# Performance work log

Measured on AMD Instinct MI355X. Metric: run time of the kernel, lower is better.

Reference implementation:

```python
import jax, jax.numpy as jnp
import numpy as np

N, E, G = 50000, 800000, 512
IN, HID, H1, H2, OUT = 128, 32, 8, 4, 128
D1, D2 = HID * H1, HID * H2  # 256, 128


def _ln(x, g, b, eps=1e-5):
    m = x.mean(-1, keepdims=True)
    v = jnp.var(x, axis=-1, keepdims=True)
    return (x - m) * jax.lax.rsqrt(v + eps) * g + b


def _gat_conv(x, W, a_src, a_dst, bias, edge_index, heads, ch, concat):
    # PyG GATConv (eval): h = xW per head; e = leakyrelu(a_src.h_src + a_dst.h_dst);
    # segment softmax over destination nodes; scatter-sum messages; self-loops added.
    n = x.shape[0]
    h = (x @ W).reshape(n, heads, ch)                      # [N,H,C]
    asrc = jnp.sum(h * a_src, axis=-1)                     # [N,H]
    adst = jnp.sum(h * a_dst, axis=-1)                     # [N,H]
    loop = jnp.arange(n)
    src = jnp.concatenate([edge_index[0], loop])           # [E+N]
    dst = jnp.concatenate([edge_index[1], loop])
    e = jax.nn.leaky_relu(asrc[src] + adst[dst], 0.2)      # [E+N,H]
    emax = jax.ops.segment_max(e, dst, num_segments=n)
    p = jnp.exp(e - emax[dst])
    denom = jax.ops.segment_sum(p, dst, num_segments=n)
    alpha = p / (denom[dst] + 1e-16)                       # [E+N,H]
    out = jax.ops.segment_sum(h[src] * alpha[..., None], dst, num_segments=n)  # [N,H,C]
    out = out.reshape(n, heads * ch) if concat else out.mean(axis=1)
    return out + bias


def setup_inputs():
    key = jax.random.key(0)
    ks = jax.random.split(key, 32)
    g = lambda i, shape, s=0.05: jax.random.normal(ks[i], shape, dtype=jnp.float32) * s
    inp = {
        "x": jax.random.normal(ks[0], (N, IN), dtype=jnp.float32),
        "edge_index": jax.random.randint(ks[1], (2, E), 0, N, dtype=jnp.int32),
        "batch": jnp.sort(jax.random.randint(ks[2], (N,), 0, G, dtype=jnp.int32)),
        # GAT layer 1: in 128 -> 8 heads x 32
        "W1": g(3, (IN, H1 * HID)), "a_src1": g(4, (H1, HID)), "a_dst1": g(5, (H1, HID)),
        "b1": jnp.zeros((D1,), jnp.float32), "g1": jnp.ones((D1,), jnp.float32), "be1": jnp.zeros((D1,), jnp.float32),
        "pw1": g(6, (IN, D1)), "pb1": jnp.zeros((D1,), jnp.float32),
        # GAT layer 2: 256 -> 4 heads x 32
        "W2": g(7, (D1, H2 * HID)), "a_src2": g(8, (H2, HID)), "a_dst2": g(9, (H2, HID)),
        "b2": jnp.zeros((D2,), jnp.float32), "g2": jnp.ones((D2,), jnp.float32), "be2": jnp.zeros((D2,), jnp.float32),
        "pw2": g(10, (D1, D2)), "pb2": jnp.zeros((D2,), jnp.float32),
        # GAT layer 3: 128 -> 1 head x 128, concat=False
        "W3": g(11, (D2, OUT)), "a_src3": g(12, (1, OUT)), "a_dst3": g(13, (1, OUT)),
        "b3": jnp.zeros((OUT,), jnp.float32), "g3": jnp.ones((OUT,), jnp.float32), "be3": jnp.zeros((OUT,), jnp.float32),
        "pw3": g(14, (D2, OUT)), "pb3": jnp.zeros((OUT,), jnp.float32),
    }
    return inp


def reference(x, edge_index, batch,
              W1, a_src1, a_dst1, b1, g1, be1, pw1, pb1,
              W2, a_src2, a_dst2, b2, g2, be2, pw2, pb2,
              W3, a_src3, a_dst3, b3, g3, be3, pw3, pb3):
    h1 = _gat_conv(x, W1, a_src1, a_dst1, b1, edge_index, H1, HID, True)
    h1 = jax.nn.elu(_ln(h1, g1, be1) + (x @ pw1 + pb1))
    h2 = _gat_conv(h1, W2, a_src2, a_dst2, b2, edge_index, H2, HID, True)
    h2 = jax.nn.elu(_ln(h2, g2, be2) + (h1 @ pw2 + pb2))
    h3 = _gat_conv(h2, W3, a_src3, a_dst3, b3, edge_index, 1, OUT, False)
    h3 = jax.nn.elu(_ln(h3, g3, be3) + (h2 @ pw3 + pb3))
    # jk='last' -> h3; global mean pool per graph
    sums = jax.ops.segment_sum(h3, batch, num_segments=G)              # [G,OUT]
    cnt = jax.ops.segment_sum(jnp.ones((N,), h3.dtype), batch, num_segments=G)
    return sums / jnp.maximum(cnt, 1.0)[:, None]
```

## Files before the change

kernel.cpp:

```cpp
#include <hip/hip_runtime.h>
#include <hip/hip_fp16.h>
#include <math.h>


typedef _Float16 f16x8 __attribute__((ext_vector_type(8)));
typedef float f32x4 __attribute__((ext_vector_type(4)));

static __device__ __forceinline__ float h2f(unsigned short u) {
  return __half2float(__builtin_bit_cast(__half, u));
}
static __device__ __forceinline__ unsigned short f2h(float f) {
  return __builtin_bit_cast(unsigned short, __float2half_rn(f));
}
static __device__ __forceinline__ float hlo(unsigned int w) {
  return __low2float(__builtin_bit_cast(__half2, w));
}
static __device__ __forceinline__ float hhi(unsigned int w) {
  return __high2float(__builtin_bit_cast(__half2, w));
}
static __device__ __forceinline__ float wave_sum(float v) {
#pragma unroll
  for (int off = 1; off < 64; off <<= 1) v += __shfl_xor(v, off, 64);
  return v;
}

template <int K, int C, int H, bool ATOMIC>
__global__ __launch_bounds__(256) void fused_gemm_kernel(
    const unsigned short* __restrict__ A, const unsigned short* __restrict__ Bp1,
    const unsigned short* __restrict__ Bp2, const float* __restrict__ bias2,
    const float* __restrict__ a_src, const float* __restrict__ a_dst,
    unsigned short* __restrict__ C1, unsigned short* __restrict__ C2,
    float* __restrict__ asrc, float* __restrict__ adst, int Ncols) {
  const int lane = threadIdx.x & 63;
  const int w = threadIdx.x >> 6;
  const int ml = lane & 15, kq = lane >> 4;
  const int row0 = blockIdx.y * 64 + (w >> 1) * 32;
  const int colt0 = blockIdx.x * 4 + (w & 1) * 2;
  constexpr int KB = K / 32;

  f32x4 w00 = {}, w01 = {}, w10 = {}, w11 = {};
  f32x4 p00 = {}, p01 = {}, p10 = {}, p11 = {};
  const unsigned short* a0 = A + (size_t)(row0 + ml) * K + kq * 8;
  const unsigned short* b1 = Bp1 + ((size_t)colt0 * KB * 64 + lane) * 8;
  const unsigned short* b2 = Bp2 + ((size_t)colt0 * KB * 64 + lane) * 8;
#pragma unroll
  for (int kb = 0; kb < KB; kb++) {
    f16x8 af0 = __builtin_bit_cast(f16x8, *(const uint4*)(a0 + kb * 32));
    f16x8 af1 = __builtin_bit_cast(f16x8, *(const uint4*)(a0 + 16 * K + kb * 32));
    f16x8 bw0 = __builtin_bit_cast(f16x8, *(const uint4*)(b1 + (size_t)kb * 512));
    f16x8 bw1 = __builtin_bit_cast(f16x8, *(const uint4*)(b1 + (size_t)(KB + kb) * 512));
    f16x8 bp0 = __builtin_bit_cast(f16x8, *(const uint4*)(b2 + (size_t)kb * 512));
    f16x8 bp1 = __builtin_bit_cast(f16x8, *(const uint4*)(b2 + (size_t)(KB + kb) * 512));
    w00 = __builtin_amdgcn_mfma_f32_16x16x32_f16(af0, bw0, w00, 0, 0, 0);
    w01 = __builtin_amdgcn_mfma_f32_16x16x32_f16(af0, bw1, w01, 0, 0, 0);
    w10 = __builtin_amdgcn_mfma_f32_16x16x32_f16(af1, bw0, w10, 0, 0, 0);
    w11 = __builtin_amdgcn_mfma_f32_16x16x32_f16(af1, bw1, w11, 0, 0, 0);
    p00 = __builtin_amdgcn_mfma_f32_16x16x32_f16(af0, bp0, p00, 0, 0, 0);
    p01 = __builtin_amdgcn_mfma_f32_16x16x32_f16(af0, bp1, p01, 0, 0, 0);
    p10 = __builtin_amdgcn_mfma_f32_16x16x32_f16(af1, bp0, p10, 0, 0, 0);
    p11 = __builtin_amdgcn_mfma_f32_16x16x32_f16(af1, bp1, p11, 0, 0, 0);
  }
  const int c0 = colt0 * 16 + ml, c1 = c0 + 16;
  const float bi0 = bias2[c0], bi1 = bias2[c1];
#pragma unroll
  for (int r = 0; r < 4; r++) {
    const size_t rA = (size_t)(row0 + kq * 4 + r);
    const size_t rB = rA + 16;
    C1[rA * Ncols + c0] = f2h(w00[r]);
    C1[rA * Ncols + c1] = f2h(w01[r]);
    C1[rB * Ncols + c0] = f2h(w10[r]);
    C1[rB * Ncols + c1] = f2h(w11[r]);
    C2[rA * Ncols + c0] = f2h(p00[r] + bi0);
    C2[rA * Ncols + c1] = f2h(p01[r] + bi1);
    C2[rB * Ncols + c0] = f2h(p10[r] + bi0);
    C2[rB * Ncols + c1] = f2h(p11[r] + bi1);
  }

  const int hh = (colt0 * 16) / C;
  const float aS0 = a_src[hh * C + (c0 % C)], aS1 = a_src[hh * C + (c1 % C)];
  const float aD0 = a_dst[hh * C + (c0 % C)], aD1 = a_dst[hh * C + (c1 % C)];
  float pS0[4], pD0[4], pS1[4], pD1[4];
#pragma unroll
  for (int r = 0; r < 4; r++) {
    pS0[r] = w00[r] * aS0 + w01[r] * aS1;
    pD0[r] = w00[r] * aD0 + w01[r] * aD1;
    pS1[r] = w10[r] * aS0 + w11[r] * aS1;
    pD1[r] = w10[r] * aD0 + w11[r] * aD1;
  }
#pragma unroll
  for (int off = 1; off < 16; off <<= 1) {
#pragma unroll
    for (int r = 0; r < 4; r++) {
      pS0[r] += __shfl_xor(pS0[r], off);
      pD0[r] += __shfl_xor(pD0[r], off);
      pS1[r] += __shfl_xor(pS1[r], off);
      pD1[r] += __shfl_xor(pD1[r], off);
    }
  }
  if (ml < 4) {
    const int r = ml;
    const int rowA = row0 + kq * 4 + r;
    const int rowB = rowA + 16;
    if constexpr (ATOMIC) {
      atomicAdd(&asrc[rowA * H + hh], pS0[r]);
      atomicAdd(&adst[rowA * H + hh], pD0[r]);
      atomicAdd(&asrc[rowB * H + hh], pS1[r]);
      atomicAdd(&adst[rowB * H + hh], pD1[r]);
    } else {
      asrc[rowA * H + hh] = pS0[r];
      adst[rowA * H + hh] = pD0[r];
      asrc[rowB * H + hh] = pS1[r];
      adst[rowB * H + hh] = pD1[r];
    }
  }
}

static __device__ __forceinline__ void repack_one(const float* B, unsigned short* Bp,
                                                  int K, int Ncols, int idx) {
  const int KB = K >> 5;
  const int lane = idx & 63;
  const int kb = (idx >> 6) % KB;
  const int nt = idx / (KB << 6);
  const int ml = lane & 15, kq = lane >> 4;
  unsigned short* dst = Bp + (size_t)idx * 8;
#pragma unroll
  for (int j = 0; j < 8; j++)
    dst[j] = f2h(B[(size_t)(kb * 32 + kq * 8 + j) * Ncols + nt * 16 + ml]);
}

__global__ __launch_bounds__(256) void repack_all_kernel(
    const float* W1, const float* pw1, const float* W2, const float* pw2,
    const float* W3, const float* pw3, unsigned short* BpW1, unsigned short* BpP1,
    unsigned short* BpW2, unsigned short* BpP2, unsigned short* BpW3,
    unsigned short* BpP3) {
  int idx = blockIdx.x * 256 + threadIdx.x;
  if (idx < 4096) { repack_one(W1, BpW1, 128, 256, idx); return; }
  idx -= 4096;
  if (idx < 4096) { repack_one(pw1, BpP1, 128, 256, idx); return; }
  idx -= 4096;
  if (idx < 4096) { repack_one(W2, BpW2, 256, 128, idx); return; }
  idx -= 4096;
  if (idx < 4096) { repack_one(pw2, BpP2, 256, 128, idx); return; }
  idx -= 4096;
  if (idx < 2048) { repack_one(W3, BpW3, 128, 128, idx); return; }
  idx -= 2048;
  repack_one(pw3, BpP3, 128, 128, idx);
}

__global__ void cast_f16_kernel(const float* __restrict__ src,
                                unsigned short* __restrict__ dst, int n4, int pad4) {
  const int i = blockIdx.x * 256 + threadIdx.x;
  if (i >= n4 + pad4) return;
  ushort4 o;
  if (i < n4) {
    float4 v = ((const float4*)src)[i];
    o.x = f2h(v.x); o.y = f2h(v.y); o.z = f2h(v.z); o.w = f2h(v.w);
  } else {
    o.x = o.y = o.z = o.w = 0;
  }
  ((ushort4*)dst)[i] = o;
}

__global__ void zero_pads_kernel(unsigned short* b256, unsigned short* b128, int pad) {
  const int i = blockIdx.x * 256 + threadIdx.x;
  if (i < pad * 256) b256[i] = 0;
  if (i < pad * 128) b128[i] = 0;
}

__global__ void zero2_kernel(float* a, float* b, int n) {
  const int i = blockIdx.x * 256 + threadIdx.x;
  if (i < n) { a[i] = 0.f; b[i] = 0.f; }
}

template <int H, int C, int SPLIT>
__global__ __launch_bounds__(256) void gat_agg_kernel(
    const unsigned short* __restrict__ hfeat, const float* __restrict__ asrc,
    const float* __restrict__ adst, const int* __restrict__ rowptr,
    const int* __restrict__ col, const float* __restrict__ bias,
    const float* __restrict__ gamma, const float* __restrict__ beta,
    const unsigned short* __restrict__ proj, unsigned short* __restrict__ out, int N) {
  constexpr int DOUT = H * C;
  constexpr int RL = DOUT / 8;
  constexpr int PD = 4;
  const int wave = threadIdx.x >> 6;
  const int lane = threadIdx.x & 63;
  const int n = blockIdx.x * 4 + wave;
  if (n >= N) return;
  const int rl = lane % RL;
  const int sub = lane / RL;
  const int c0 = rl * 8;
  const int myh = c0 / C;
  const int start = rowptr[n];
  const int deg = rowptr[n + 1] - start;
  const int vlen = deg + 1;
  const float my_adl = adst[n * H + myh];

  float acc[8];
#pragma unroll
  for (int i = 0; i < 8; i++) acc[i] = 0.f;
  float psum = 0.f;
  const __half2 hz = __float2half2_rn(0.f);

  for (int chunk = 0; chunk < vlen; chunk += 64) {
    const int loc = chunk + lane;
    const int cv = (loc < deg) ? col[start + loc] : n;
    const int m = min(64, vlen - chunk);
    const int steps = (m + SPLIT - 1) / SPLIT;
    const int ngroups = (steps + PD - 1) / PD;

    __half2 acc2[4] = {hz, hz, hz, hz};
    float aA[PD], aB[PD];
    uint4 hA[PD], hB[PD];

#pragma unroll
    for (int k = 0; k < PD; k++) {
      const int local = k * SPLIT + sub;
      int s = __shfl(cv, local & 63);
      if (local >= m) s = n;
      aA[k] = asrc[s * H + myh];
      hA[k] = *(const uint4*)&hfeat[(size_t)s * DOUT + c0];
    }
    for (int g = 0; g < ngroups; g += 2) {
      if (g + 1 < ngroups) {
#pragma unroll
        for (int k = 0; k < PD; k++) {
          const int local = ((g + 1) * PD + k) * SPLIT + sub;
          int s = __shfl(cv, local & 63);
          if (local >= m) s = n;
          aB[k] = asrc[s * H + myh];
          hB[k] = *(const uint4*)&hfeat[(size_t)s * DOUT + c0];
        }
      }
#pragma unroll
      for (int k = 0; k < PD; k++) {
        const int local = (g * PD + k) * SPLIT + sub;
        float e = aA[k] + my_adl;
        e = (e > 0.f) ? e : 0.2f * e;
        float p = __expf(e);
        p = (local < m) ? p : 0.f;
        psum += p;
        const __half2 pp = __float2half2_rn(p);
        acc2[0] = __hfma2(__builtin_bit_cast(__half2, hA[k].x), pp, acc2[0]);
        acc2[1] = __hfma2(__builtin_bit_cast(__half2, hA[k].y), pp, acc2[1]);
        acc2[2] = __hfma2(__builtin_bit_cast(__half2, hA[k].z), pp, acc2[2]);
        acc2[3] = __hfma2(__builtin_bit_cast(__half2, hA[k].w), pp, acc2[3]);
      }
      if (g + 1 < ngroups) {
        if (g + 2 < ngroups) {
#pragma unroll
          for (int k = 0; k < PD; k++) {
            const int local = ((g + 2) * PD + k) * SPLIT + sub;
            int s = __shfl(cv, local & 63);
            if (local >= m) s = n;
            aA[k] = asrc[s * H + myh];
            hA[k] = *(const uint4*)&hfeat[(size_t)s * DOUT + c0];
          }
        }
#pragma unroll
        for (int k = 0; k < PD; k++) {
          const int local = ((g + 1) * PD + k) * SPLIT + sub;
          float e = aB[k] + my_adl;
          e = (e > 0.f) ? e : 0.2f * e;
          float p = __expf(e);
          p = (local < m) ? p : 0.f;
          psum += p;
          const __half2 pp = __float2half2_rn(p);
          acc2[0] = __hfma2(__builtin_bit_cast(__half2, hB[k].x), pp, acc2[0]);
          acc2[1] = __hfma2(__builtin_bit_cast(__half2, hB[k].y), pp, acc2[1]);
          acc2[2] = __hfma2(__builtin_bit_cast(__half2, hB[k].z), pp, acc2[2]);
          acc2[3] = __hfma2(__builtin_bit_cast(__half2, hB[k].w), pp, acc2[3]);
        }
      }
    }
#pragma unroll
    for (int i = 0; i < 4; i++) {
      acc[2 * i] += __low2float(acc2[i]);
      acc[2 * i + 1] += __high2float(acc2[i]);
    }
  }

#pragma unroll
  for (int o = RL; o < 64; o <<= 1) {
    psum += __shfl_xor(psum, o);
#pragma unroll
    for (int i = 0; i < 8; i++) acc[i] += __shfl_xor(acc[i], o);
  }

  const float rs = 1.f / (psum + 1e-16f);
  const float4 bi0 = *(const float4*)&bias[c0];
  const float4 bi1 = *(const float4*)&bias[c0 + 4];
  float v[8];
  v[0] = acc[0] * rs + bi0.x; v[1] = acc[1] * rs + bi0.y;
  v[2] = acc[2] * rs + bi0.z; v[3] = acc[3] * rs + bi0.w;
  v[4] = acc[4] * rs + bi1.x; v[5] = acc[5] * rs + bi1.y;
  v[6] = acc[6] * rs + bi1.z; v[7] = acc[7] * rs + bi1.w;

  float s8 = 0.f;
#pragma unroll
  for (int i = 0; i < 8; i++) s8 += v[i];
  const float mean = wave_sum(s8) / (float)(DOUT * SPLIT);
  float q8 = 0.f;
#pragma unroll
  for (int i = 0; i < 8; i++) {
    v[i] -= mean;
    q8 += v[i] * v[i];
  }
  const float var = wave_sum(q8) / (float)(DOUT * SPLIT);
  const float rstd = rsqrtf(var + 1e-5f);

  const float4 ga0 = *(const float4*)&gamma[c0];
  const float4 ga1 = *(const float4*)&gamma[c0 + 4];
  const float4 be0 = *(const float4*)&beta[c0];
  const float4 be1 = *(const float4*)&beta[c0 + 4];
  const uint4 pr = *(const uint4*)&proj[(size_t)n * DOUT + c0];
  float o0 = v[0] * rstd * ga0.x + be0.x + hlo(pr.x);
  float o1 = v[1] * rstd * ga0.y + be0.y + hhi(pr.x);
  float o2 = v[2] * rstd * ga0.z + be0.z + hlo(pr.y);
  float o3 = v[3] * rstd * ga0.w + be0.w + hhi(pr.y);
  float o4 = v[4] * rstd * ga1.x + be1.x + hlo(pr.z);
  float o5 = v[5] * rstd * ga1.y + be1.y + hhi(pr.z);
  float o6 = v[6] * rstd * ga1.z + be1.z + hlo(pr.w);
  float o7 = v[7] * rstd * ga1.w + be1.w + hhi(pr.w);
  o0 = (o0 > 0.f) ? o0 : expm1f(o0);
  o1 = (o1 > 0.f) ? o1 : expm1f(o1);
  o2 = (o2 > 0.f) ? o2 : expm1f(o2);
  o3 = (o3 > 0.f) ? o3 : expm1f(o3);
  o4 = (o4 > 0.f) ? o4 : expm1f(o4);
  o5 = (o5 > 0.f) ? o5 : expm1f(o5);
  o6 = (o6 > 0.f) ? o6 : expm1f(o6);
  o7 = (o7 > 0.f) ? o7 : expm1f(o7);
  if (sub == 0) {
    uint4 ov;
    ov.x = (unsigned int)f2h(o0) | ((unsigned int)f2h(o1) << 16);
    ov.y = (unsigned int)f2h(o2) | ((unsigned int)f2h(o3) << 16);
    ov.z = (unsigned int)f2h(o4) | ((unsigned int)f2h(o5) << 16);
    ov.w = (unsigned int)f2h(o6) | ((unsigned int)f2h(o7) << 16);
    *(uint4*)&out[(size_t)n * DOUT + c0] = ov;
  }
}

__global__ void hist_kernel(const int* __restrict__ dst, int* __restrict__ cnt, int E) {
  const int e = blockIdx.x * 256 + threadIdx.x;
  if (e < E) atomicAdd(&cnt[dst[e]], 1);
}

__global__ __launch_bounds__(256) void scan1_kernel(int* __restrict__ cnt,
                                                    int* __restrict__ sums, int N) {
  __shared__ int sm[256];
  const int i = blockIdx.x * 256 + threadIdx.x;
  const int v = (i < N) ? cnt[i] : 0;
  sm[threadIdx.x] = v;
  __syncthreads();
  for (int off = 1; off < 256; off <<= 1) {
    const int t = (threadIdx.x >= off) ? sm[threadIdx.x - off] : 0;
    __syncthreads();
    sm[threadIdx.x] += t;
    __syncthreads();
  }
  if (i < N) cnt[i] = sm[threadIdx.x] - v;
  if (threadIdx.x == 255) sums[blockIdx.x] = sm[255];
}

__global__ __launch_bounds__(256) void scan2_kernel(int* __restrict__ sums, int nb) {
  __shared__ int sm[256];
  const int v = (threadIdx.x < nb) ? sums[threadIdx.x] : 0;
  sm[threadIdx.x] = v;
  __syncthreads();
  for (int off = 1; off < 256; off <<= 1) {
    const int t = (threadIdx.x >= off) ? sm[threadIdx.x - off] : 0;
    __syncthreads();
    sm[threadIdx.x] += t;
    __syncthreads();
  }
  if (threadIdx.x < nb) sums[threadIdx.x] = sm[threadIdx.x] - v;
}

__global__ void scan3_kernel(const int* __restrict__ cnt, const int* __restrict__ sums,
                             int* __restrict__ rowptr, int* __restrict__ cursor,
                             int N, int E) {
  const int i = blockIdx.x * 256 + threadIdx.x;
  if (i < N) {
    const int r = cnt[i] + sums[blockIdx.x];
    rowptr[i] = r;
    cursor[i] = r;
  }
  if (i == 0) rowptr[N] = E;
}

__global__ void scatter_kernel(const int* __restrict__ src, const int* __restrict__ dst,
                               int* __restrict__ cursor, int* __restrict__ col, int E) {
  const int e = blockIdx.x * 256 + threadIdx.x;
  if (e < E) {
    const int p = atomicAdd(&cursor[dst[e]], 1);
    col[p] = src[e];
  }
}

__global__ __launch_bounds__(128) void pool_kernel(const unsigned short* __restrict__ h3,
                                                   const int* __restrict__ batch,
                                                   float* __restrict__ out, int N) {
  __shared__ int sse[2];
  const int g = blockIdx.x;
  if (threadIdx.x == 0) {
    int lo = 0, hi = N;
    while (lo < hi) { const int mid = (lo + hi) >> 1; if (batch[mid] < g) lo = mid + 1; else hi = mid; }
    sse[0] = lo;
    lo = 0; hi = N;
    while (lo < hi) { const int mid = (lo + hi) >> 1; if (batch[mid] < g + 1) lo = mid + 1; else hi = mid; }
    sse[1] = lo;
  }
  __syncthreads();
  const int s = sse[0], e = sse[1];
  float sum = 0.f;
  for (int r = s; r < e; r++) sum += h2f(h3[(size_t)r * 128 + threadIdx.x]);
  out[g * 128 + threadIdx.x] = (e > s) ? sum / (float)(e - s) : 0.f;
}

extern "C" void kernel_launch(void* const* d_in, const int* in_sizes, int n_in,
                              void* d_out, int out_size, void* d_ws, size_t ws_size,
                              hipStream_t stream) {
  const float* x      = (const float*)d_in[0];
  const int* edge_idx = (const int*)d_in[1];
  const int* batch    = (const int*)d_in[2];
  const float* W1     = (const float*)d_in[3];
  const float* a_src1 = (const float*)d_in[4];
  const float* a_dst1 = (const float*)d_in[5];
  const float* b1     = (const float*)d_in[6];
  const float* g1     = (const float*)d_in[7];
  const float* be1    = (const float*)d_in[8];
  const float* pw1    = (const float*)d_in[9];
  const float* pb1    = (const float*)d_in[10];
  const float* W2     = (const float*)d_in[11];
  const float* a_src2 = (const float*)d_in[12];
  const float* a_dst2 = (const float*)d_in[13];
  const float* b2     = (const float*)d_in[14];
  const float* g2     = (const float*)d_in[15];
  const float* be2    = (const float*)d_in[16];
  const float* pw2    = (const float*)d_in[17];
  const float* pb2    = (const float*)d_in[18];
  const float* W3     = (const float*)d_in[19];
  const float* a_src3 = (const float*)d_in[20];
  const float* a_dst3 = (const float*)d_in[21];
  const float* b3     = (const float*)d_in[22];
  const float* g3     = (const float*)d_in[23];
  const float* be3    = (const float*)d_in[24];
  const float* pw3    = (const float*)d_in[25];
  const float* pb3    = (const float*)d_in[26];

  const int NN = in_sizes[0] / 128;
  const int E  = in_sizes[1] / 2;
  const int G  = out_size / 128;
  const int M64 = (NN + 63) & ~63;

  size_t off = 0;
  auto alloc = [&](size_t bytes) {
    size_t r = off;
    off += (bytes + 255) & ~(size_t)255;
    return r;
  };
  char* ws = (char*)d_ws;
  unsigned short* big0 = (unsigned short*)(ws + alloc((size_t)M64 * 256 * 2));
  unsigned short* big1 = (unsigned short*)(ws + alloc((size_t)M64 * 256 * 2));
  unsigned short* s0   = (unsigned short*)(ws + alloc((size_t)M64 * 128 * 2));
  unsigned short* s1   = (unsigned short*)(ws + alloc((size_t)M64 * 128 * 2));
  unsigned short* projb = (unsigned short*)(ws + alloc((size_t)M64 * 256 * 2));
  float* asrcB = (float*)(ws + alloc((size_t)M64 * 8 * 4));
  float* adstB = (float*)(ws + alloc((size_t)M64 * 8 * 4));
  int* rowptr  = (int*)(ws + alloc((size_t)(NN + 1) * 4));
  int* cnt     = (int*)(ws + alloc((size_t)NN * 4));
  int* cursor  = (int*)(ws + alloc((size_t)NN * 4));
  int* colb    = (int*)(ws + alloc((size_t)E * 4));
  int* sums    = (int*)(ws + alloc(256 * 4));
  unsigned short* BpW1 = (unsigned short*)(ws + alloc(128 * 256 * 2));
  unsigned short* BpP1 = (unsigned short*)(ws + alloc(128 * 256 * 2));
  unsigned short* BpW2 = (unsigned short*)(ws + alloc(256 * 128 * 2));
  unsigned short* BpP2 = (unsigned short*)(ws + alloc(256 * 128 * 2));
  unsigned short* BpW3 = (unsigned short*)(ws + alloc(128 * 128 * 2));
  unsigned short* BpP3 = (unsigned short*)(ws + alloc(128 * 128 * 2));
  (void)ws_size; (void)n_in;

  const int EB = (E + 255) / 256;
  const int NB = (NN + 255) / 256;
  const int NW = (NN + 3) / 4;
  const int MB = M64 / 64;
  const int pad = M64 - NN;

  hipMemsetAsync(cnt, 0, (size_t)NN * 4, stream);
  hist_kernel<<<EB, 256, 0, stream>>>(edge_idx + E, cnt, E);
  scan1_kernel<<<NB, 256, 0, stream>>>(cnt, sums, NN);
  scan2_kernel<<<1, 256, 0, stream>>>(sums, NB);
  scan3_kernel<<<NB, 256, 0, stream>>>(cnt, sums, rowptr, cursor, NN, E);
  scatter_kernel<<<EB, 256, 0, stream>>>(edge_idx, edge_idx + E, cursor, colb, E);

  cast_f16_kernel<<<(M64 * 128 / 4 + 255) / 256, 256, 0, stream>>>(x, s0, NN * 32, pad * 32);
  if (pad)
    zero_pads_kernel<<<(pad * 256 + 255) / 256, 256, 0, stream>>>(
        big1 + (size_t)NN * 256, s1 + (size_t)NN * 128, pad);

  repack_all_kernel<<<80, 256, 0, stream>>>(W1, pw1, W2, pw2, W3, pw3,
                                            BpW1, BpP1, BpW2, BpP2, BpW3, BpP3);

  fused_gemm_kernel<128, 32, 8, false><<<dim3(4, MB), 256, 0, stream>>>(
      s0, BpW1, BpP1, pb1, a_src1, a_dst1, big0, projb, asrcB, adstB, 256);
  gat_agg_kernel<8, 32, 2><<<NW, 256, 0, stream>>>(big0, asrcB, adstB, rowptr, colb,
                                                   b1, g1, be1, projb, big1, NN);

  fused_gemm_kernel<256, 32, 4, false><<<dim3(2, MB), 256, 0, stream>>>(
      big1, BpW2, BpP2, pb2, a_src2, a_dst2, s0, projb, asrcB, adstB, 128);
  gat_agg_kernel<4, 32, 4><<<NW, 256, 0, stream>>>(s0, asrcB, adstB, rowptr, colb,
                                                   b2, g2, be2, projb, s1, NN);

  zero2_kernel<<<(M64 + 255) / 256, 256, 0, stream>>>(asrcB, adstB, M64);
  fused_gemm_kernel<128, 128, 1, true><<<dim3(2, MB), 256, 0, stream>>>(
      s1, BpW3, BpP3, pb3, a_src3, a_dst3, big0, projb, asrcB, adstB, 128);
  gat_agg_kernel<1, 128, 4><<<NW, 256, 0, stream>>>(big0, asrcB, adstB, rowptr, colb,
                                                    b3, g3, be3, projb, s0, NN);

  pool_kernel<<<G, 128, 0, stream>>>(s0, batch, (float*)d_out, NN);
}
```

Before: 498.1 us.

## Widen per-lane feature slice to 16 halves and gather neighbor indices directly

Each lane in the GAT aggregation kernel now handles 16 feature channels (two 16-byte loads) instead of 8, so more neighbors are processed in parallel per wave (SPLIT doubled). The 64-wide chunk loop with shuffle-broadcast of column indices is replaced by direct per-lane loads of col entries across the whole neighbor list, with a single fp16 accumulator set and no per-chunk flush to fp32. The prefetch depth drops from 4 to 2, and ELU now uses __expf minus 1 instead of expm1f. In exchange, registers per lane rise and half-precision accumulation runs over the full degree, which may cost accuracy.

Result: slower. 508.9 us (+2.2%).

```diff
diff --git a/kernel.cpp b/kernel.cpp
--- a/kernel.cpp
+++ b/kernel.cpp
@@ -180,162 +180,145 @@
     const float* __restrict__ gamma, const float* __restrict__ beta,
     const unsigned short* __restrict__ proj, unsigned short* __restrict__ out, int N) {
   constexpr int DOUT = H * C;
-  constexpr int RL = DOUT / 8;
-  constexpr int PD = 4;
+  constexpr int RL = DOUT / 16;
+  static_assert(RL * SPLIT == 64, "bad split");
+  constexpr int PD = 2;
   const int wave = threadIdx.x >> 6;
   const int lane = threadIdx.x & 63;
   const int n = blockIdx.x * 4 + wave;
   if (n >= N) return;
   const int rl = lane % RL;
   const int sub = lane / RL;
-  const int c0 = rl * 8;
+  const int c0 = rl * 16;
   const int myh = c0 / C;
   const int start = rowptr[n];
   const int deg = rowptr[n + 1] - start;
   const int vlen = deg + 1;
+  const int nsteps = (vlen + SPLIT - 1) / SPLIT;
+  const int ngroups = (nsteps + PD - 1) / PD;
   const float my_adl = adst[n * H + myh];
-
-  float acc[8];
-#pragma unroll
-  for (int i = 0; i < 8; i++) acc[i] = 0.f;
+  const int clmax = (deg > 0) ? deg - 1 : 0;
+
+  const __half2 hz = __float2half2_rn(0.f);
+  __half2 acc2[8] = {hz, hz, hz, hz, hz, hz, hz, hz};
   float psum = 0.f;
-  const __half2 hz = __float2half2_rn(0.f);
-
-  for (int chunk = 0; chunk < vlen; chunk += 64) {
-    const int loc = chunk + lane;
-    const int cv = (loc < deg) ? col[start + loc] : n;
-    const int m = min(64, vlen - chunk);
-    const int steps = (m + SPLIT - 1) / SPLIT;
-    const int ngroups = (steps + PD - 1) / PD;
-
-    __half2 acc2[4] = {hz, hz, hz, hz};
-    float aA[PD], aB[PD];
-    uint4 hA[PD], hB[PD];
-
+
+  float aA[PD], aB[PD];
+  uint4 h0A[PD], h1A[PD], h0B[PD], h1B[PD];
+
+  auto issue = [&](int g, float* a, uint4* h0, uint4* h1) {
 #pragma unroll
     for (int k = 0; k < PD; k++) {
-      const int local = k * SPLIT + sub;
-      int s = __shfl(cv, local & 63);
-      if (local >= m) s = n;
-      aA[k] = asrc[s * H + myh];
-      hA[k] = *(const uint4*)&hfeat[(size_t)s * DOUT + c0];
+      const int j = (g * PD + k) * SPLIT + sub;
+      int s = col[start + min(j, clmax)];
+      s = (j < deg) ? s : n;
+      a[k] = asrc[s * H + myh];
+      const unsigned short* hp = &hfeat[(size_t)s * DOUT + c0];
+      h0[k] = *(const uint4*)hp;
+      h1[k] = *(const uint4*)(hp + 8);
     }
-    for (int g = 0; g < ngroups; g += 2) {
-      if (g + 1 < ngroups) {
-#pragma unroll
-        for (int k = 0; k < PD; k++) {
-          const int local = ((g + 1) * PD + k) * SPLIT + sub;
-          int s = __shfl(cv, local & 63);
-          if (local >= m) s = n;
-          aB[k] = asrc[s * H + myh];
-          hB[k] = *(const uint4*)&hfeat[(size_t)s * DOUT + c0];
-        }
-      }
-#pragma unroll
-      for (int k = 0; k < PD; k++) {
-        const int local = (g * PD + k) * SPLIT + sub;
-        float e = aA[k] + my_adl;
-        e = (e > 0.f) ? e : 0.2f * e;
-        float p = __expf(e);
-        p = (local < m) ? p : 0.f;
-        psum += p;
-        const __half2 pp = __float2half2_rn(p);
-        acc2[0] = __hfma2(__builtin_bit_cast(__half2, hA[k].x), pp, acc2[0]);
-        acc2[1] = __hfma2(__builtin_bit_cast(__half2, hA[k].y), pp, acc2[1]);
-        acc2[2] = __hfma2(__builtin_bit_cast(__half2, hA[k].z), pp, acc2[2]);
-        acc2[3] = __hfma2(__builtin_bit_cast(__half2, hA[k].w), pp, acc2[3]);
-      }
-      if (g + 1 < ngroups) {
-        if (g + 2 < ngroups) {
-#pragma unroll
-          for (int k = 0; k < PD; k++) {
-            const int local = ((g + 2) * PD + k) * SPLIT + sub;
-            int s = __shfl(cv, local & 63);
-            if (local >= m) s = n;
-            aA[k] = asrc[s * H + myh];
-            hA[k] = *(const uint4*)&hfeat[(size_t)s * DOUT + c0];
-          }
-        }
-#pragma unroll
-        for (int k = 0; k < PD; k++) {
-          const int local = ((g + 1) * PD + k) * SPLIT + sub;
-          float e = aB[k] + my_adl;
-          e = (e > 0.f) ? e : 0.2f * e;
-          float p = __expf(e);
-          p = (local < m) ? p : 0.f;
-          psum += p;
-          const __half2 pp = __float2half2_rn(p);
-          acc2[0] = __hfma2(__builtin_bit_cast(__half2, hB[k].x), pp, acc2[0]);
-          acc2[1] = __hfma2(__builtin_bit_cast(__half2, hB[k].y), pp, acc2[1]);
-          acc2[2] = __hfma2(__builtin_bit_cast(__half2, hB[k].z), pp, acc2[2]);
-          acc2[3] = __hfma2(__builtin_bit_cast(__half2, hB[k].w), pp, acc2[3]);
-        }
-      }
+  };
+  auto consume = [&](int g, const float* a, const uint4* h0, const uint4* h1) {
+#pragma unroll
+    for (int k = 0; k < PD; k++) {
+      const int j = (g * PD + k) * SPLIT + sub;
+      float e = a[k] + my_adl;
+      e = fmaxf(e, 0.2f * e);
+      float p = __expf(e);
+      p = (j < vlen) ? p : 0.f;
+      psum += p;
+      const __half2 pp = __float2half2_rn(p);
+      acc2[0] = __hfma2(__builtin_bit_cast(__half2, h0[k].x), pp, acc2[0]);
+      acc2[1] = __hfma2(__builtin_bit_cast(__half2, h0[k].y), pp, acc2[1]);
+      acc2[2] = __hfma2(__builtin_bit_cast(__half2, h0[k].z), pp, acc2[2]);
+      acc2[3] = __hfma2(__builtin_bit_cast(__half2, h0[k].w), pp, acc2[3]);
+      acc2[4] = __hfma2(__builtin_bit_cast(__half2, h1[k].x), pp, acc2[4]);
+      acc2[5] = __hfma2(__builtin_bit_cast(__half2, h1[k].y), pp, acc2[5]);
+      acc2[6] = __hfma2(__builtin_bit_cast(__half2, h1[k].z), pp, acc2[6]);
+      acc2[7] = __hfma2(__builtin_bit_cast(__half2, h1[k].w), pp, acc2[7]);
     }
-#pragma unroll
-    for (int i = 0; i < 4; i++) {
-      acc[2 * i] += __low2float(acc2[i]);
-      acc[2 * i + 1] += __high2float(acc2[i]);
+  };
+
+  issue(0, aA, h0A, h1A);
+  for (int g = 0; g < ngroups; g += 2) {
+    if (g + 1 < ngroups) issue(g + 1, aB, h0B, h1B);
+    consume(g, aA, h0A, h1A);
+    if (g + 1 < ngroups) {
+      if (g + 2 < ngroups) issue(g + 2, aA, h0A, h1A);
+      consume(g + 1, aB, h0B, h1B);
     }
   }
 
+  float acc[16];
+#pragma unroll
+  for (int i = 0; i < 8; i++) {
+    acc[2 * i] = __low2float(acc2[i]);
+    acc[2 * i + 1] = __high2float(acc2[i]);
+  }
 #pragma unroll
   for (int o = RL; o < 64; o <<= 1) {
     psum += __shfl_xor(psum, o);
 #pragma unroll
-    for (int i = 0; i < 8; i++) acc[i] += __shfl_xor(acc[i], o);
+    for (int i = 0; i < 16; i++) acc[i] += __shfl_xor(acc[i], o);
   }
 
   const float rs = 1.f / (psum + 1e-16f);
-  const float4 bi0 = *(const float4*)&bias[c0];
-  const float4 bi1 = *(const float4*)&bias[c0 + 4];
-  float v[8];
-  v[0] = acc[0] * rs + bi0.x; v[1] = acc[1] * rs + bi0.y;
-  v[2] = acc[2] * rs + bi0.z; v[3] = acc[3] * rs + bi0.w;
-  v[4] = acc[4] * rs + bi1.x; v[5] = acc[5] * rs + bi1.y;
-  v[6] = acc[6] * rs + bi1.z; v[7] = acc[7] * rs + bi1.w;
-
-  float s8 = 0.f;
-#pragma unroll
-  for (int i = 0; i < 8; i++) s8 += v[i];
-  const float mean = wave_sum(s8) / (float)(DOUT * SPLIT);
-  float q8 = 0.f;
-#pragma unroll
-  for (int i = 0; i < 8; i++) {
+  float v[16];
+#pragma unroll
+  for (int q = 0; q < 4; q++) {
+    const float4 bi = *(const float4*)&bias[c0 + q * 4];
+    v[q * 4 + 0] = acc[q * 4 + 0] * rs + bi.x;
+    v[q * 4 + 1] = acc[q * 4 + 1] * rs + bi.y;
+    v[q * 4 + 2] = acc[q * 4 + 2] * rs + bi.z;
+    v[q * 4 + 3] = acc[q * 4 + 3] * rs + bi.w;
+  }
+  float s16 = 0.f;
+#pragma unroll
+  for (int i = 0; i < 16; i++) s16 += v[i];
+  const float mean = wave_sum(s16) / (float)(DOUT * SPLIT);
+  float q16 = 0.f;
+#pragma unroll
+  for (int i = 0; i < 16; i++) {
     v[i] -= mean;
-    q8 += v[i] * v[i];
-  }
-  const float var = wave_sum(q8) / (float)(DOUT * SPLIT);
+    q16 += v[i] * v[i];
+  }
+  const float var = wave_sum(q16) / (float)(DOUT * SPLIT);
   const float rstd = rsqrtf(var + 1e-5f);
 
-  const float4 ga0 = *(const float4*)&gamma[c0];
-  const float4 ga1 = *(const float4*)&gamma[c0 + 4];
-  const float4 be0 = *(const float4*)&beta[c0];
-  const float4 be1 = *(const float4*)&beta[c0 + 4];
-  const uint4 pr = *(const uint4*)&proj[(size_t)n * DOUT + c0];
-  float o0 = v[0] * rstd * ga0.x + be0.x + hlo(pr.x);
-  float o1 = v[1] * rstd * ga0.y + be0.y + hhi(pr.x);
-  float o2 = v[2] * rstd * ga0.z + be0.z + hlo(pr.y);
-  float o3 = v[3] * rstd * ga0.w + be0.w + hhi(pr.y);
-  float o4 = v[4] * rstd * ga1.x + be1.x + hlo(pr.z);
-  float o5 = v[5] * rstd * ga1.y + be1.y + hhi(pr.z);
-  float o6 = v[6] * rstd * ga1.z + be1.z + hlo(pr.w);
-  float o7 = v[7] * rstd * ga1.w + be1.w + hhi(pr.w);
-  o0 = (o0 > 0.f) ? o0 : expm1f(o0);
-  o1 = (o1 > 0.f) ? o1 : expm1f(o1);
-  o2 = (o2 > 0.f) ? o2 : expm1f(o2);
-  o3 = (o3 > 0.f) ? o3 : expm1f(o3);
-  o4 = (o4 > 0.f) ? o4 : expm1f(o4);
-  o5 = (o5 > 0.f) ? o5 : expm1f(o5);
-  o6 = (o6 > 0.f) ? o6 : expm1f(o6);
-  o7 = (o7 > 0.f) ? o7 : expm1f(o7);
+  const uint4 pr0 = *(const uint4*)&proj[(size_t)n * DOUT + c0];
+  const uint4 pr1 = *(const uint4*)&proj[(size_t)n * DOUT + c0 + 8];
+  float pres[16];
+  pres[0] = hlo(pr0.x); pres[1] = hhi(pr0.x); pres[2] = hlo(pr0.y); pres[3] = hhi(pr0.y);
+  pres[4] = hlo(pr0.z); pres[5] = hhi(pr0.z); pres[6] = hlo(pr0.w); pres[7] = hhi(pr0.w);
+  pres[8] = hlo(pr1.x); pres[9] = hhi(pr1.x); pres[10] = hlo(pr1.y); pres[11] = hhi(pr1.y);
+  pres[12] = hlo(pr1.z); pres[13] = hhi(pr1.z); pres[14] = hlo(pr1.w); pres[15] = hhi(pr1.w);
+
+  float o16[16];
+#pragma unroll
+  for (int q = 0; q < 4; q++) {
+    const float4 ga = *(const float4*)&gamma[c0 + q * 4];
+    const float4 be = *(const float4*)&beta[c0 + q * 4];
+    o16[q * 4 + 0] = v[q * 4 + 0] * rstd * ga.x + be.x + pres[q * 4 + 0];
+    o16[q * 4 + 1] = v[q * 4 + 1] * rstd * ga.y + be.y + pres[q * 4 + 1];
+    o16[q * 4 + 2] = v[q * 4 + 2] * rstd * ga.z + be.z + pres[q * 4 + 2];
+    o16[q * 4 + 3] = v[q * 4 + 3] * rstd * ga.w + be.w + pres[q * 4 + 3];
+  }
+#pragma unroll
+  for (int i = 0; i < 16; i++)
+    o16[i] = (o16[i] > 0.f) ? o16[i] : (__expf(o16[i]) - 1.f);
+
   if (sub == 0) {
-    uint4 ov;
-    ov.x = (unsigned int)f2h(o0) | ((unsigned int)f2h(o1) << 16);
-    ov.y = (unsigned int)f2h(o2) | ((unsigned int)f2h(o3) << 16);
-    ov.z = (unsigned int)f2h(o4) | ((unsigned int)f2h(o5) << 16);
-    ov.w = (unsigned int)f2h(o6) | ((unsigned int)f2h(o7) << 16);
-    *(uint4*)&out[(size_t)n * DOUT + c0] = ov;
+    uint4 ov0, ov1;
+    ov0.x = (unsigned int)f2h(o16[0]) | ((unsigned int)f2h(o16[1]) << 16);
+    ov0.y = (unsigned int)f2h(o16[2]) | ((unsigned int)f2h(o16[3]) << 16);
+    ov0.z = (unsigned int)f2h(o16[4]) | ((unsigned int)f2h(o16[5]) << 16);
+    ov0.w = (unsigned int)f2h(o16[6]) | ((unsigned int)f2h(o16[7]) << 16);
+    ov1.x = (unsigned int)f2h(o16[8]) | ((unsigned int)f2h(o16[9]) << 16);
+    ov1.y = (unsigned int)f2h(o16[10]) | ((unsigned int)f2h(o16[11]) << 16);
+    ov1.z = (unsigned int)f2h(o16[12]) | ((unsigned int)f2h(o16[13]) << 16);
+    ov1.w = (unsigned int)f2h(o16[14]) | ((unsigned int)f2h(o16[15]) << 16);
+    *(uint4*)&out[(size_t)n * DOUT + c0] = ov0;
+    *(uint4*)&out[(size_t)n * DOUT + c0 + 8] = ov1;
   }
 }
 
@@ -469,7 +452,7 @@
   int* rowptr  = (int*)(ws + alloc((size_t)(NN + 1) * 4));
   int* cnt     = (int*)(ws + alloc((size_t)NN * 4));
   int* cursor  = (int*)(ws + alloc((size_t)NN * 4));
-  int* colb    = (int*)(ws + alloc((size_t)E * 4));
+  int* colb    = (int*)(ws + alloc((size_t)(E + 64) * 4));
   int* sums    = (int*)(ws + alloc(256 * 4));
   unsigned short* BpW1 = (unsigned short*)(ws + alloc(128 * 256 * 2));
   unsigned short* BpP1 = (unsigned short*)(ws + alloc(128 * 256 * 2));
@@ -502,18 +485,18 @@
 
   fused_gemm_kernel<128, 32, 8, false><<<dim3(4, MB), 256, 0, stream>>>(
       s0, BpW1, BpP1, pb1, a_src1, a_dst1, big0, projb, asrcB, adstB, 256);
-  gat_agg_kernel<8, 32, 2><<<NW, 256, 0, stream>>>(big0, asrcB, adstB, rowptr, colb,
+  gat_agg_kernel<8, 32, 4><<<NW, 256, 0, stream>>>(big0, asrcB, adstB, rowptr, colb,
                                                    b1, g1, be1, projb, big1, NN);
 
   fused_gemm_kernel<256, 32, 4, false><<<dim3(2, MB), 256, 0, stream>>>(
       big1, BpW2, BpP2, pb2, a_src2, a_dst2, s0, projb, asrcB, adstB, 128);
-  gat_agg_kernel<4, 32, 4><<<NW, 256, 0, stream>>>(s0, asrcB, adstB, rowptr, colb,
+  gat_agg_kernel<4, 32, 8><<<NW, 256, 0, stream>>>(s0, asrcB, adstB, rowptr, colb,
                                                    b2, g2, be2, projb, s1, NN);
 
   zero2_kernel<<<(M64 + 255) / 256, 256, 0, stream>>>(asrcB, adstB, M64);
   fused_gemm_kernel<128, 128, 1, true><<<dim3(2, MB), 256, 0, stream>>>(
       s1, BpW3, BpP3, pb3, a_src3, a_dst3, big0, projb, asrcB, adstB, 128);
-  gat_agg_kernel<1, 128, 4><<<NW, 256, 0, stream>>>(big0, asrcB, adstB, rowptr, colb,
+  gat_agg_kernel<1, 128, 8><<<NW, 256, 0, stream>>>(big0, asrcB, adstB, rowptr, colb,
                                                     b3, g3, be3, projb, s0, NN);
 
   pool_kernel<<<G, 128, 0, stream>>>(s0, batch, (float*)d_out, NN);
```
